# Kernel tuning notes

Hardware: AMD Instinct MI355X
Metric: run time of the kernel (lower is better)

## Reference

```python
import jax, jax.numpy as jnp
import numpy as np

N_QUBITS = 12
DIM = 2 ** N_QUBITS
N_RES_LAYERS = 3
N_HEADS = 2
N_ATTN_LAYERS = 2
SEQ_LEN = 64
HORIZON = 4
BATCH = 8
N_PARAMS = N_QUBITS * 2 * N_ATTN_LAYERS  # 48
FEAT = N_QUBITS * N_HEADS  # 24

# ---- static (numpy) precomputed gate structures (little-endian, qiskit convention) ----
_idx = np.arange(DIM)

def _cx_perm(c, t):
    # CNOT: flip target bit where control bit is 1 -> index permutation
    return np.where(((_idx >> c) & 1) == 1, _idx ^ (1 << t), _idx)

def _cz_phase(a, b):
    return (1.0 - 2.0 * (((_idx >> a) & 1) * ((_idx >> b) & 1))).astype(np.float32)

CX_LADDER = [jnp.asarray(_cx_perm(i, i + 1)) for i in range(N_QUBITS - 1)]
CX_RING = jnp.asarray(_cx_perm(N_QUBITS - 1, 0))
CX_LONG = jnp.asarray(_cx_perm(0, N_QUBITS - 1))
_CZ = []
for _layer in range(N_RES_LAYERS):
    _ph = np.ones(DIM, np.float32)
    for _i in range(_layer % 2, N_QUBITS - 1, 2):
        _ph *= _cz_phase(_i, _i + 1)
    _CZ.append(jnp.asarray(_ph))
# Qiskit Pauli label 'I'*i + 'Z' + 'I'*(n-i-1) acts on qubit n-1-i (big-endian labels)
Z_SIGNS = jnp.asarray(np.stack([
    (1.0 - 2.0 * ((_idx >> (N_QUBITS - 1 - i)) & 1)).astype(np.float32)
    for i in range(N_QUBITS)]))  # (n, DIM)


def _apply_1q(state, gate, q):
    # state: (..., DIM); gate: (2,2) or (...,2,2) broadcastable against leading dims
    hi = DIM >> (q + 1)
    lo = 1 << q
    s = state.reshape(state.shape[:-1] + (hi, 2, lo))
    out = jnp.einsum('...ij,...hjl->...hil', gate, s)
    return out.reshape(state.shape)


def _ry(theta):
    c = jnp.cos(theta / 2)
    s = jnp.sin(theta / 2)
    g = jnp.stack([jnp.stack([c, -s], -1), jnp.stack([s, c], -1)], -2)
    return g.astype(jnp.complex64)


def _rz(phi):
    em = jnp.exp(-0.5j * phi)
    ep = jnp.exp(0.5j * phi)
    z = jnp.zeros_like(em)
    return jnp.stack([jnp.stack([em, z], -1), jnp.stack([z, ep], -1)], -2)


def _u3(t, p, l):
    ct = jnp.cos(t / 2).astype(jnp.complex64)
    st = jnp.sin(t / 2).astype(jnp.complex64)
    return jnp.stack([jnp.stack([ct, -jnp.exp(1j * l) * st]),
                      jnp.stack([jnp.exp(1j * p) * st, jnp.exp(1j * (p + l)) * ct])])


def _encode_reservoir(x, res_params):
    # x: (B,T) normalized scalars -> batched statevectors (B,T,DIM)
    B, T = x.shape
    # H^{\otimes n} |0...0> = uniform superposition
    state = jnp.full((B, T, DIM), 1.0 / np.sqrt(DIM), jnp.complex64)
    for i in range(N_QUBITS):
        state = _apply_1q(state, _ry(x * np.pi * (i + 1) / N_QUBITS), i)
        state = _apply_1q(state, _rz(x * np.pi / (i + 1)), i)
    for p in CX_LADDER:
        state = state[..., p]
    state = state[..., CX_RING]
    # fixed random reservoir
    for layer in range(N_RES_LAYERS):
        for i in range(N_QUBITS):
            g = _u3(res_params[layer, i, 0], res_params[layer, i, 1], res_params[layer, i, 2])
            state = _apply_1q(state, g, i)
        state = state * _CZ[layer]
        state = state[..., CX_LONG]  # n > 2
    return state


def _project(state, params):
    # projection circuit: per layer RY/RZ on each qubit then CNOT ladder; then <Z_i>
    for layer in range(N_ATTN_LAYERS):
        for i in range(N_QUBITS):
            k = (layer * N_QUBITS + i) * 2
            state = _apply_1q(state, _ry(params[k]), i)
            state = _apply_1q(state, _rz(params[k + 1]), i)
        for p in CX_LADDER:
            state = state[..., p]
    probs = state.real ** 2 + state.imag ** 2  # (B,T,DIM)
    return jnp.einsum('btd,qd->btq', probs, Z_SIGNS)  # (B,T,n)


def setup_inputs() -> dict:
    key = jax.random.key(0)
    ks = jax.random.split(key, 6)
    sequence = jax.random.uniform(ks[0], (BATCH, SEQ_LEN), jnp.float32)
    res_params = jax.random.uniform(ks[1], (N_RES_LAYERS, N_QUBITS, 3), jnp.float32,
                                    minval=0.0, maxval=2.0 * np.pi)
    head_params = jax.random.uniform(ks[2], (N_HEADS, 3, N_PARAMS), jnp.float32,
                                     minval=0.0, maxval=2.0 * np.pi)
    W1 = jax.random.normal(ks[3], (FEAT, 2 * FEAT), jnp.float32) / np.sqrt(FEAT)
    b1 = jnp.zeros((2 * FEAT,), jnp.float32)
    W2 = jax.random.normal(ks[4], (2 * FEAT, HORIZON), jnp.float32) / np.sqrt(2 * FEAT)
    b2 = jnp.zeros((HORIZON,), jnp.float32)
    return {'sequence': sequence, 'res_params': res_params, 'head_params': head_params,
            'W1': W1, 'b1': b1, 'W2': W2, 'b2': b2}


def reference(sequence, res_params, head_params, W1, b1, W2, b2):
    states = _encode_reservoir(sequence, res_params)  # (B,T,DIM)
    T = sequence.shape[1]
    mask = jnp.triu(jnp.full((T, T), -1e9, jnp.float32), k=1)
    outs = []
    for h in range(N_HEADS):
        Q = _project(states, head_params[h, 0])
        K = _project(states, head_params[h, 1])
        V = _project(states, head_params[h, 2])
        scores = jnp.einsum('btd,bsd->bts', Q, K) / np.sqrt(N_QUBITS) + mask
        attn = jax.nn.softmax(scores, axis=-1)
        outs.append(jnp.einsum('bts,bsd->btd', attn, V))
    feats = jnp.concatenate(outs, -1)  # (B,T,FEAT)
    last = feats[:, -1, :]
    hdn = jax.nn.gelu(last @ W1 + b1, approximate=False)  # torch GELU default = exact erf
    pred = hdn @ W2 + b2  # (B, HORIZON)
    return pred
```

## Files before the change

### kernel.cpp

```cpp
#include <hip/hip_runtime.h>
#include <hip/hip_bf16.h>


#define PADDED 4224
#define HPAD   2112

#define LDSFENCE asm volatile("s_waitcnt lgkmcnt(0)" ::: "memory")

__device__ __forceinline__ int PD(int j) { return j + (j >> 5); }
__device__ __forceinline__ int PH(int i) { return i + (i >> 5); }

__device__ __forceinline__ int mapIdx(int j, int mode) {
  if (mode == 1) { int k = j ^ ((j >> 11) & 1); return k ^ ((k & 0x7FF) << 1); }
  if (mode == 2) { return j ^ ((j & 1) << 11); }
  if (mode == 3) { return j ^ ((j & 0x7FF) << 1); }
  return j;
}

template <int L>
__device__ __forceinline__ int layoutIdx(int tid, int r) {
  if constexpr (L == 0) return (tid << 4) | r;
  else if constexpr (L == 1) return ((tid & 0xF0) << 4) | (r << 4) | (tid & 15);
  else if constexpr (L == 2) return (r << 8) | tid;
  else return ((tid & 15) << 8) | (tid & 0xF0) | r;
}

template <int B>
__device__ __forceinline__ int dropbit(int j) {
  constexpr int lo = (1 << B) - 1;
  return (j & lo) | ((j >> 1) & ~lo);
}

template <int L>
__device__ __forceinline__ void ldsRead16(const float* sR, const float* sI, int tid, int mode,
                                          float ar[16], float ai[16]) {
#pragma unroll
  for (int r = 0; r < 16; ++r) {
    int j = layoutIdx<L>(tid, r);
    int a = PD(mapIdx(j, mode));
    ar[r] = sR[a]; ai[r] = sI[a];
  }
}

template <int L>
__device__ __forceinline__ void ldsWrite16(float* sR, float* sI, int tid,
                                           const float ar[16], const float ai[16], int czmask) {
#pragma unroll
  for (int r = 0; r < 16; ++r) {
    int j = layoutIdx<L>(tid, r);
    float vr = ar[r], vi = ai[r];
    if (czmask) {
      float sg = (__popc((j & (j >> 1)) & czmask) & 1) ? -1.0f : 1.0f;
      vr *= sg; vi *= sg;
    }
    int a = PD(j);
    sR[a] = vr; sI[a] = vi;
  }
}

template <int L, int B>
__device__ __forceinline__ void hWrite16(float* hR, float* hI, int tid,
                                         const float ar[16], const float ai[16]) {
#pragma unroll
  for (int r = 0; r < 16; ++r) {
    int j = layoutIdx<L>(tid, r);
    int a = PH(dropbit<B>(j));
    hR[a] = ar[r]; hI[a] = ai[r];
  }
}

template <int L, int B, int MODE>
__device__ __forceinline__ void hRead16(const float* hR, const float* hI, int tid,
                                        float ar[16], float ai[16]) {
#pragma unroll
  for (int r = 0; r < 16; ++r) {
    int j = mapIdx(layoutIdx<L>(tid, r), MODE);
    int a = PH(dropbit<B>(j));
    ar[r] = hR[a]; ai[r] = hI[a];
  }
}

__device__ __forceinline__ void applyU34(float ar[16], float ai[16], const float (*ut)[8]) {
#pragma unroll
  for (int b = 0; b < 4; ++b) {
    const float* u = ut[b];
    float u00r = u[0];
    float u01r = u[2], u01i = u[3];
    float u10r = u[4], u10i = u[5], u11r = u[6], u11i = u[7];
#pragma unroll
    for (int m = 0; m < 8; ++m) {
      int p0 = ((m >> b) << (b + 1)) | (m & ((1 << b) - 1));
      int p1 = p0 | (1 << b);
      float x0r = ar[p0], x0i = ai[p0], x1r = ar[p1], x1i = ai[p1];
      ar[p0] = u00r * x0r + u01r * x1r - u01i * x1i;
      ai[p0] = u00r * x0i + u01r * x1i + u01i * x1r;
      ar[p1] = u10r * x0r - u10i * x0i + u11r * x1r - u11i * x1i;
      ai[p1] = u10r * x0i + u10i * x0r + u11r * x1i + u11i * x1r;
    }
  }
}

__device__ __forceinline__ void applyRyRz4(float ar[16], float ai[16], const float4* gt) {
#pragma unroll
  for (int b = 0; b < 4; ++b) {
    float4 g = gt[b];
    float c = g.x, s = g.y, zr = g.z, zi = g.w;
#pragma unroll
    for (int m = 0; m < 8; ++m) {
      int p0 = ((m >> b) << (b + 1)) | (m & ((1 << b) - 1));
      int p1 = p0 | (1 << b);
      float x0r = ar[p0], x0i = ai[p0], x1r = ar[p1], x1i = ai[p1];
      float n0r = c * x0r - s * x1r;
      float n0i = c * x0i - s * x1i;
      float wr  = s * x0r + c * x1r;
      float wi  = s * x0i + c * x1i;
      ar[p0] = n0r;              ai[p0] = n0i;
      ar[p1] = wr * zr - wi * zi; ai[p1] = wr * zi + wi * zr;
    }
  }
}

template <int L>
__device__ __forceinline__ void encPass(float* sR, float* sI, int tid, int mode,
                                        const float (*ut)[8], int czmask) {
  float ar[16], ai[16];
  ldsRead16<L>(sR, sI, tid, mode, ar, ai);
  if (mode != 0) __syncthreads();
  applyU34(ar, ai, ut);
  ldsWrite16<L>(sR, sI, tid, ar, ai, czmask);
  __syncthreads();
}

template <int L>
__device__ __forceinline__ void projPass(float* sR, float* sI, int tid, int mode, const float4* gt) {
  float ar[16], ai[16];
  ldsRead16<L>(sR, sI, tid, mode, ar, ai);
  if (mode != 0) __syncthreads();
  applyRyRz4(ar, ai, gt);
  ldsWrite16<L>(sR, sI, tid, ar, ai, 0);
  __syncthreads();
}

__device__ __forceinline__ void projFinal(const float* sR, const float* sI, int tid,
                                          const float4* gt, float feat[12]) {
  float ar[16], ai[16];
#pragma unroll
  for (int r = 0; r < 16; ++r) {
    int a = PD((r << 8) | tid);
    ar[r] = sR[a]; ai[r] = sI[a];
  }
  applyRyRz4(ar, ai, gt);
  float sp = 0.f, f0 = 0.f, f1 = 0.f, f2 = 0.f, f3 = 0.f;
  int pt = __popc(tid) & 1;
#pragma unroll
  for (int r = 0; r < 16; ++r) {
    float p = ar[r] * ar[r] + ai[r] * ai[r];
    sp += p;
    int tr = r ^ (r << 1); tr ^= (tr << 2);
    f0 += ((pt ^ ((tr >> 3) & 1)) ? -p : p);
    f1 += ((pt ^ ((tr >> 2) & 1)) ? -p : p);
    f2 += ((pt ^ ((tr >> 1) & 1)) ? -p : p);
    f3 += ((pt ^ (tr & 1)) ? -p : p);
  }
  feat[0] = f0; feat[1] = f1; feat[2] = f2; feat[3] = f3;
  int tt = tid ^ (tid << 1); tt ^= (tt << 2); tt ^= (tt << 4);
#pragma unroll
  for (int q = 4; q < 12; ++q)
    feat[q] = ((tt >> (11 - q)) & 1) ? -sp : sp;
}

__device__ __forceinline__ float waveReduce(float v) {
#pragma unroll
  for (int off = 32; off; off >>= 1) v += __shfl_xor(v, off, 64);
  return v;
}


__device__ __forceinline__ void buildQtab(float4* qtab, int tid, float x) {
  const float PI = 3.14159265358979323846f;
  const float RS2 = 0.70710678118654752440f;
  if (tid < 12) {
    int i = tid;
    float th = x * PI * (float)(i + 1) / 12.0f;
    float ph = x * PI / (float)(i + 1);
    float s, c;  sincosf(0.5f * th, &s, &c);
    float zi, zr; sincosf(0.5f * ph, &zi, &zr);
    float k0 = (c - s) * RS2, k1 = (c + s) * RS2;
    qtab[i] = make_float4(k0 * zr, -k0 * zi, k1 * zr, k1 * zi);
  }
}

__device__ __forceinline__ void buildUtab(float (*utab)[8], int tid, const float* resp) {
  if (tid >= 64 && tid < 100) {
    int i = tid - 64;
    const float* rp = resp + i * 3;
    float st, ct;  sincosf(0.5f * rp[0], &st, &ct);
    float sp2, cp; sincosf(rp[1], &sp2, &cp);
    float sl, cl;  sincosf(rp[2], &sl, &cl);
    float spl, cpl; sincosf(rp[1] + rp[2], &spl, &cpl);
    float* u = utab[i];
    u[0] = ct;       u[1] = 0.0f;
    u[2] = -cl * st; u[3] = -sl * st;
    u[4] = cp * st;  u[5] = sp2 * st;
    u[6] = cpl * ct; u[7] = spl * ct;
  }
}

__device__ __forceinline__ void initProduct(float* sRe, float* sIm, int tid, const float4* qtab) {
  float pr, pi;
  {
    float4 g = qtab[4];
    int sb = tid & 1;
    pr = sb ? g.z : g.x; pi = sb ? g.w : g.y;
  }
#pragma unroll
  for (int q = 5; q < 12; ++q) {
    float4 g = qtab[q];
    int sb = (tid >> (q - 4)) & 1;
    float fr = sb ? g.z : g.x, fi = sb ? g.w : g.y;
    float nr = pr * fr - pi * fi;
    pi = pr * fi + pi * fr; pr = nr;
  }
  float4 g0 = qtab[0], g1 = qtab[1], g2 = qtab[2], g3 = qtab[3];
  float c01r[4], c01i[4], c23r[4], c23i[4];
#pragma unroll
  for (int i2 = 0; i2 < 4; ++i2) {
    float f0r = (i2 & 1) ? g0.z : g0.x, f0i = (i2 & 1) ? g0.w : g0.y;
    float f1r = (i2 & 2) ? g1.z : g1.x, f1i = (i2 & 2) ? g1.w : g1.y;
    c01r[i2] = f0r * f1r - f0i * f1i; c01i[i2] = f0r * f1i + f0i * f1r;
    float f2r = (i2 & 1) ? g2.z : g2.x, f2i = (i2 & 1) ? g2.w : g2.y;
    float f3r = (i2 & 2) ? g3.z : g3.x, f3i = (i2 & 2) ? g3.w : g3.y;
    c23r[i2] = f2r * f3r - f2i * f3i; c23i[i2] = f2r * f3i + f2i * f3r;
  }
#pragma unroll
  for (int r = 0; r < 16; ++r) {
    float lr = c01r[r & 3] * c23r[r >> 2] - c01i[r & 3] * c23i[r >> 2];
    float li = c01r[r & 3] * c23i[r >> 2] + c01i[r & 3] * c23r[r >> 2];
    int a = PD((tid << 4) | r);
    sRe[a] = pr * lr - pi * li;
    sIm[a] = pr * li + pi * lr;
  }
}

__device__ __forceinline__ void buildPtab(float4* ptab, int tid, const float* hp) {
  if (tid < 24) {
    int k = tid * 2;
    float s, c;  sincosf(0.5f * hp[k], &s, &c);
    float zi, zr; sincosf(hp[k + 1], &zi, &zr);
    ptab[tid] = make_float4(c, s, zr, zi);
  }
}


__global__ __launch_bounds__(256, 2) void enc_kernel(
    const float* __restrict__ seq, const float* __restrict__ resp,
    float* __restrict__ wsStates) {
  __shared__ float sRe[PADDED], sIm[PADDED];
  __shared__ float4 qtab[12];
  __shared__ float utab[36][8];

  const int tid = threadIdx.x;
  const int blk = blockIdx.x;
  const float x = seq[blk];

  buildQtab(qtab, tid, x);
  buildUtab(utab, tid, resp);
  __syncthreads();

  initProduct(sRe, sIm, tid, qtab);
  __syncthreads();

  encPass<0>(sRe, sIm, tid, 1, &utab[0], 0);
  encPass<1>(sRe, sIm, tid, 0, &utab[4], 0);
  encPass<2>(sRe, sIm, tid, 0, &utab[8], 0x555);
  encPass<0>(sRe, sIm, tid, 2, &utab[12], 0);
  encPass<1>(sRe, sIm, tid, 0, &utab[16], 0);
  encPass<2>(sRe, sIm, tid, 0, &utab[20], 0x2AA);
  encPass<0>(sRe, sIm, tid, 2, &utab[24], 0);
  encPass<1>(sRe, sIm, tid, 0, &utab[28], 0);

  {
    float ar[16], ai[16];
    ldsRead16<2>(sRe, sIm, tid, 0, ar, ai);
    applyU34(ar, ai, &utab[32]);
    float* gR = wsStates + (size_t)blk * 8192;
    float* gI = gR + 4096;
#pragma unroll
    for (int r = 0; r < 16; ++r) {
      int j = (r << 8) | tid;
      float sg = (__popc((j & (j >> 1)) & 0x555) & 1) ? -1.0f : 1.0f;
      int g = j ^ ((j & 1) << 11);
      gR[g] = sg * ar[r];
      gI[g] = sg * ai[r];
    }
  }
}

__global__ __launch_bounds__(256, 5) void proj_split(
    const float* __restrict__ wsStates, const float* __restrict__ hparams,
    float* __restrict__ featBase) {
  __shared__ float hRe[HPAD], hIm[HPAD];
  __shared__ float4 ptab[24];
  __shared__ float red[4][12];

  const int tid = threadIdx.x;
  const int bid = blockIdx.x;
  int h, which, s;
  if (bid < 2048) { s = bid >> 2; int pp = bid & 3; h = pp >> 1; which = 1 + (pp & 1); }
  else            { int i = bid - 2048; h = i & 1; s = (((i >> 1) << 6) | 63); which = 0; }
  const int b = s >> 6, t = s & 63;

  buildPtab(ptab, tid, hparams + (h * 3 + which) * 48);

  float ar[16], ai[16];
  const float4* pR = (const float4*)(wsStates + (size_t)s * 8192 + (tid << 4));
  const float4* pI = (const float4*)(wsStates + (size_t)s * 8192 + 4096 + (tid << 4));
#pragma unroll
  for (int k = 0; k < 4; ++k) {
    float4 vr = pR[k], vi = pI[k];
    ar[4 * k] = vr.x; ar[4 * k + 1] = vr.y; ar[4 * k + 2] = vr.z; ar[4 * k + 3] = vr.w;
    ai[4 * k] = vi.x; ai[4 * k + 1] = vi.y; ai[4 * k + 2] = vi.z; ai[4 * k + 3] = vi.w;
  }
  __syncthreads();

  const int ph7 = (tid >> 7) & 1;
  const int ph3 = (tid >> 3) & 1;
  const int ph0 = tid & 1;

  applyRyRz4(ar, ai, &ptab[0]);

  if (ph7 == 0) { hWrite16<0, 11>(hRe, hIm, tid, ar, ai); LDSFENCE; hRead16<1, 11, 0>(hRe, hIm, tid, ar, ai); }
  __syncthreads();
  if (ph7 == 1) { hWrite16<0, 11>(hRe, hIm, tid, ar, ai); LDSFENCE; hRead16<1, 11, 0>(hRe, hIm, tid, ar, ai); }

  applyRyRz4(ar, ai, &ptab[4]);

  __syncthreads();
  if (ph3 == 0) hWrite16<1, 3>(hRe, hIm, tid, ar, ai);
  __syncthreads();
  if (ph3 == 0) hRead16<2, 3, 0>(hRe, hIm, tid, ar, ai);
  __syncthreads();
  if (ph3 == 1) hWrite16<1, 3>(hRe, hIm, tid, ar, ai);
  __syncthreads();
  if (ph3 == 1) hRead16<2, 3, 0>(hRe, hIm, tid, ar, ai);

  applyRyRz4(ar, ai, &ptab[8]);

  __syncthreads();
  if (ph0 == 0) hWrite16<2, 0>(hRe, hIm, tid, ar, ai);
  __syncthreads();
  if (ph0 == 0) hRead16<1, 0, 3>(hRe, hIm, tid, ar, ai);
  __syncthreads();
  if (ph0 == 1) hWrite16<2, 0>(hRe, hIm, tid, ar, ai);
  __syncthreads();
  if (ph0 == 1) hRead16<1, 0, 3>(hRe, hIm, tid, ar, ai);

  applyRyRz4(ar, ai, &ptab[16]);

  __syncthreads();
  if (ph3 == 0) hWrite16<1, 3>(hRe, hIm, tid, ar, ai);
  __syncthreads();
  if (ph3 == 0) hRead16<2, 3, 0>(hRe, hIm, tid, ar, ai);
  __syncthreads();
  if (ph3 == 1) hWrite16<1, 3>(hRe, hIm, tid, ar, ai);
  __syncthreads();
  if (ph3 == 1) hRead16<2, 3, 0>(hRe, hIm, tid, ar, ai);

  applyRyRz4(ar, ai, &ptab[20]);

  __syncthreads();
  if (ph7 == 0) { hWrite16<2, 7>(hRe, hIm, tid, ar, ai); LDSFENCE; hRead16<3, 7, 0>(hRe, hIm, tid, ar, ai); }
  __syncthreads();
  if (ph7 == 1) { hWrite16<2, 7>(hRe, hIm, tid, ar, ai); LDSFENCE; hRead16<3, 7, 0>(hRe, hIm, tid, ar, ai); }

  applyRyRz4(ar, ai, &ptab[12]);
  float A = 0.f, B2 = 0.f, B1 = 0.f, B0 = 0.f;
#pragma unroll
  for (int r = 0; r < 16; ++r) {
    float p = ar[r] * ar[r] + ai[r] * ai[r];
    int tr = r ^ (r << 1); tr ^= (tr << 2);
    A  += ((tr >> 3) & 1) ? -p : p;
    B2 += ((tr >> 2) & 1) ? -p : p;
    B1 += ((tr >> 1) & 1) ? -p : p;
    B0 += ((tr & 1)      ) ? -p : p;
  }
  int t03p = __popc(tid & 0x0F) & 1;
  int t47p = __popc(tid & 0xF0) & 1;
  int u4   = (tid >> 4) & 1;
  int u45  = u4 ^ ((tid >> 5) & 1);
  int u456 = u45 ^ ((tid >> 6) & 1);
  int v0   = tid & 1;
  int v01  = v0 ^ ((tid >> 1) & 1);
  int v012 = v01 ^ ((tid >> 2) & 1);
  float feat[12];
  feat[0]  = (t47p ^ t03p) ? -A : A;
  feat[1]  = (t47p ^ v012) ? -A : A;
  feat[2]  = (t47p ^ v01)  ? -A : A;
  feat[3]  = (t47p ^ v0)   ? -A : A;
  feat[4]  = t47p ? -A : A;
  feat[5]  = u456 ? -A : A;
  feat[6]  = u45  ? -A : A;
  feat[7]  = u4   ? -A : A;
  feat[8]  = A;
  feat[9]  = B2;
  feat[10] = B1;
  feat[11] = B0;

#pragma unroll
  for (int q = 0; q < 12; ++q) feat[q] = waveReduce(feat[q]);
  int wid = tid >> 6;
  if ((tid & 63) == 0) {
#pragma unroll
    for (int q = 0; q < 12; ++q) red[wid][q] = feat[q];
  }
  __syncthreads();
  if (tid < 12) {
    float v = red[0][tid] + red[1][tid] + red[2][tid] + red[3][tid];
    float* dst;
    if (which == 1)      dst = featBase + (((h << 3) + b) * 64 + t) * 12;
    else if (which == 2) dst = featBase + 12288 + (((h << 3) + b) * 64 + t) * 12;
    else                 dst = featBase + 24576 + ((h << 3) + b) * 12;
    dst[tid] = v;
  }
}


__global__ __launch_bounds__(256, 2) void qstates_mono(
    const float* __restrict__ seq, const float* __restrict__ resp,
    const float* __restrict__ hparams, float* __restrict__ featBase) {
  __shared__ float sRe[PADDED], sIm[PADDED];
  __shared__ float4 qtab[12];
  __shared__ float utab[36][8];
  __shared__ float4 ptab[24];
  __shared__ float red[4][12];

  const int tid = threadIdx.x;
  const int blk = blockIdx.x;
  const int b = blk >> 6;
  const int t = blk & 63;
  const float x = seq[blk];

  buildQtab(qtab, tid, x);
  buildUtab(utab, tid, resp);
  __syncthreads();
  initProduct(sRe, sIm, tid, qtab);
  __syncthreads();

  for (int l = 0; l < 3; ++l) {
    int czm = (l & 1) ? 0x2AA : 0x555;
    encPass<0>(sRe, sIm, tid, (l == 0) ? 1 : 2, &utab[l * 12], 0);
    encPass<1>(sRe, sIm, tid, 0, &utab[l * 12 + 4], 0);
    encPass<2>(sRe, sIm, tid, 0, &utab[l * 12 + 8], czm);
  }

  float encR[16], encI[16];
#pragma unroll
  for (int r = 0; r < 16; ++r) {
    int j = (tid << 4) | r;
    int a = PD(j ^ ((j & 1) << 11));
    encR[r] = sRe[a]; encI[r] = sIm[a];
  }

  const int nproj = (t == 63) ? 6 : 4;
  for (int pj = 0; pj < nproj; ++pj) {
    int h, which;
    if (pj < 4) { h = pj >> 1; which = (pj & 1) ? 2 : 1; }
    else        { h = pj - 4;  which = 0; }
    buildPtab(ptab, tid, hparams + (h * 3 + which) * 48);
    __syncthreads();

    float ar[16], ai[16];
#pragma unroll
    for (int r = 0; r < 16; ++r) { ar[r] = encR[r]; ai[r] = encI[r]; }
    applyRyRz4(ar, ai, &ptab[0]);
    ldsWrite16<0>(sRe, sIm, tid, ar, ai, 0);
    __syncthreads();
    projPass<1>(sRe, sIm, tid, 0, &ptab[4]);
    projPass<2>(sRe, sIm, tid, 0, &ptab[8]);
    projPass<0>(sRe, sIm, tid, 3, &ptab[12]);
    projPass<1>(sRe, sIm, tid, 0, &ptab[16]);

    float feat[12];
    projFinal(sRe, sIm, tid, &ptab[20], feat);
#pragma unroll
    for (int q = 0; q < 12; ++q) feat[q] = waveReduce(feat[q]);
    int wid = tid >> 6;
    if ((tid & 63) == 0) {
#pragma unroll
      for (int q = 0; q < 12; ++q) red[wid][q] = feat[q];
    }
    __syncthreads();
    if (tid < 12) {
      float v = red[0][tid] + red[1][tid] + red[2][tid] + red[3][tid];
      float* dst;
      if (which == 1)      dst = featBase + (((h << 3) + b) * 64 + t) * 12;
      else if (which == 2) dst = featBase + 12288 + (((h << 3) + b) * 64 + t) * 12;
      else                 dst = featBase + 24576 + ((h << 3) + b) * 12;
      dst[tid] = v;
    }
    __syncthreads();
  }
}


__global__ __launch_bounds__(64) void qhead_kernel(
    const float* __restrict__ featBase,
    const float* __restrict__ W1, const float* __restrict__ b1,
    const float* __restrict__ W2, const float* __restrict__ b2,
    float* __restrict__ out) {
  __shared__ float feats[24];
  __shared__ float hdn[48];
  const int b = blockIdx.x;
  const int lane = threadIdx.x;
  const float* Kf = featBase;
  const float* Vf = featBase + 12288;
  const float* Qf = featBase + 24576;
  for (int h = 0; h < 2; ++h) {
    const float* q  = Qf + ((h << 3) + b) * 12;
    const float* kr = Kf + ((((h << 3) + b) << 6) + lane) * 12;
    float dot = 0.f;
#pragma unroll
    for (int d = 0; d < 12; ++d) dot += q[d] * kr[d];
    dot *= 0.288675134594812882f;
    float mx = dot;
#pragma unroll
    for (int off = 32; off; off >>= 1) mx = fmaxf(mx, __shfl_xor(mx, off, 64));
    float e = expf(dot - mx);
    float se = e;
#pragma unroll
    for (int off = 32; off; off >>= 1) se += __shfl_xor(se, off, 64);
    float a = e / se;
    const float* vr = Vf + ((((h << 3) + b) << 6) + lane) * 12;
#pragma unroll
    for (int d = 0; d < 12; ++d) {
      float v = a * vr[d];
#pragma unroll
      for (int off = 32; off; off >>= 1) v += __shfl_xor(v, off, 64);
      if (lane == 0) feats[h * 12 + d] = v;
    }
  }
  __syncthreads();
  if (lane < 48) {
    float acc = b1[lane];
#pragma unroll
    for (int f = 0; f < 24; ++f) acc += feats[f] * W1[f * 48 + lane];
    hdn[lane] = 0.5f * acc * (1.0f + erff(acc * 0.70710678118654752440f));
  }
  __syncthreads();
  if (lane < 4) {
    float acc = b2[lane];
#pragma unroll
    for (int k = 0; k < 48; ++k) acc += hdn[k] * W2[k * 4 + lane];
    out[(b << 2) | lane] = acc;
  }
}

extern "C" void kernel_launch(void* const* d_in, const int* in_sizes, int n_in,
                              void* d_out, int out_size, void* d_ws, size_t ws_size,
                              hipStream_t stream) {
  const float* seq     = (const float*)d_in[0];
  const float* resp    = (const float*)d_in[1];
  const float* hparams = (const float*)d_in[2];
  const float* W1      = (const float*)d_in[3];
  const float* b1      = (const float*)d_in[4];
  const float* W2      = (const float*)d_in[5];
  const float* b2      = (const float*)d_in[6];
  float* out = (float*)d_out;
  float* ws  = (float*)d_ws;

  const size_t needSplit = ((size_t)512 * 8192 + 24768) * sizeof(float);
  if (ws_size >= needSplit) {
    float* wsStates = ws;
    float* featBase = ws + (size_t)512 * 8192;
    hipLaunchKernelGGL(enc_kernel, dim3(512), dim3(256), 0, stream, seq, resp, wsStates);
    hipLaunchKernelGGL(proj_split, dim3(2064), dim3(256), 0, stream, wsStates, hparams, featBase);
    hipLaunchKernelGGL(qhead_kernel, dim3(8), dim3(64), 0, stream, featBase, W1, b1, W2, b2, out);
  } else {
    hipLaunchKernelGGL(qstates_mono, dim3(512), dim3(256), 0, stream, seq, resp, hparams, ws);
    hipLaunchKernelGGL(qhead_kernel, dim3(8), dim3(64), 0, stream, ws, W1, b1, W2, b2, out);
  }
}
```

Baseline: 165.8 us.

## Use 512 threads with 3-qubit passes in reservoir encoding kernel

```diff
diff --git a/kernel.cpp b/kernel.cpp
--- a/kernel.cpp
+++ b/kernel.cpp
@@ -25,6 +25,14 @@
   else return ((tid & 15) << 8) | (tid & 0xF0) | r;
 }
 
+template <int K>
+__device__ __forceinline__ int layoutIdx3(int tid, int r) {
+  constexpr int S = 3 * K;
+  int lo = tid & ((1 << S) - 1);
+  int hi = tid >> S;
+  return (hi << (S + 3)) | (r << S) | lo;
+}
+
 template <int B>
 __device__ __forceinline__ int dropbit(int j) {
   constexpr int lo = (1 << B) - 1;
@@ -89,6 +97,26 @@
     float u10r = u[4], u10i = u[5], u11r = u[6], u11i = u[7];
 #pragma unroll
     for (int m = 0; m < 8; ++m) {
+      int p0 = ((m >> b) << (b + 1)) | (m & ((1 << b) - 1));
+      int p1 = p0 | (1 << b);
+      float x0r = ar[p0], x0i = ai[p0], x1r = ar[p1], x1i = ai[p1];
+      ar[p0] = u00r * x0r + u01r * x1r - u01i * x1i;
+      ai[p0] = u00r * x0i + u01r * x1i + u01i * x1r;
+      ar[p1] = u10r * x0r - u10i * x0i + u11r * x1r - u11i * x1i;
+      ai[p1] = u10r * x0i + u10i * x0r + u11r * x1i + u11i * x1r;
+    }
+  }
+}
+
+__device__ __forceinline__ void applyU3_3(float ar[8], float ai[8], const float (*ut)[8]) {
+#pragma unroll
+  for (int b = 0; b < 3; ++b) {
+    const float* u = ut[b];
+    float u00r = u[0];
+    float u01r = u[2], u01i = u[3];
+    float u10r = u[4], u10i = u[5], u11r = u[6], u11i = u[7];
+#pragma unroll
+    for (int m = 0; m < 4; ++m) {
       int p0 = ((m >> b) << (b + 1)) | (m & ((1 << b) - 1));
       int p1 = p0 | (1 << b);
       float x0r = ar[p0], x0i = ai[p0], x1r = ar[p1], x1i = ai[p1];
@@ -131,13 +159,29 @@
   __syncthreads();
 }
 
-template <int L>
-__device__ __forceinline__ void projPass(float* sR, float* sI, int tid, int mode, const float4* gt) {
-  float ar[16], ai[16];
-  ldsRead16<L>(sR, sI, tid, mode, ar, ai);
+template <int K>
+__device__ __forceinline__ void encPass3(float* sR, float* sI, int tid, int mode,
+                                         const float (*ut)[8], int czmask) {
+  float ar[8], ai[8];
+#pragma unroll
+  for (int r = 0; r < 8; ++r) {
+    int j = layoutIdx3<K>(tid, r);
+    int a = PD(mapIdx(j, mode));
+    ar[r] = sR[a]; ai[r] = sI[a];
+  }
   if (mode != 0) __syncthreads();
-  applyRyRz4(ar, ai, gt);
-  ldsWrite16<L>(sR, sI, tid, ar, ai, 0);
+  applyU3_3(ar, ai, ut);
+#pragma unroll
+  for (int r = 0; r < 8; ++r) {
+    int j = layoutIdx3<K>(tid, r);
+    float vr = ar[r], vi = ai[r];
+    if (czmask) {
+      float sg = (__popc((j & (j >> 1)) & czmask) & 1) ? -1.0f : 1.0f;
+      vr *= sg; vi *= sg;
+    }
+    int a = PD(j);
+    sR[a] = vr; sI[a] = vi;
+  }
   __syncthreads();
 }
 
@@ -242,6 +286,40 @@
   }
 }
 
+__device__ __forceinline__ void initProduct3(float* sRe, float* sIm, int tid, const float4* qtab) {
+  float pr, pi;
+  {
+    float4 g = qtab[3];
+    int sb = tid & 1;
+    pr = sb ? g.z : g.x; pi = sb ? g.w : g.y;
+  }
+#pragma unroll
+  for (int q = 4; q < 12; ++q) {
+    float4 g = qtab[q];
+    int sb = (tid >> (q - 3)) & 1;
+    float fr = sb ? g.z : g.x, fi = sb ? g.w : g.y;
+    float nr = pr * fr - pi * fi;
+    pi = pr * fi + pi * fr; pr = nr;
+  }
+  float4 g0 = qtab[0], g1 = qtab[1], g2 = qtab[2];
+  float c01r[4], c01i[4];
+#pragma unroll
+  for (int i2 = 0; i2 < 4; ++i2) {
+    float f0r = (i2 & 1) ? g0.z : g0.x, f0i = (i2 & 1) ? g0.w : g0.y;
+    float f1r = (i2 & 2) ? g1.z : g1.x, f1i = (i2 & 2) ? g1.w : g1.y;
+    c01r[i2] = f0r * f1r - f0i * f1i; c01i[i2] = f0r * f1i + f0i * f1r;
+  }
+#pragma unroll
+  for (int r = 0; r < 8; ++r) {
+    float f2r = (r & 4) ? g2.z : g2.x, f2i = (r & 4) ? g2.w : g2.y;
+    float lr = c01r[r & 3] * f2r - c01i[r & 3] * f2i;
+    float li = c01r[r & 3] * f2i + c01i[r & 3] * f2r;
+    int a = PD((tid << 3) | r);
+    sRe[a] = pr * lr - pi * li;
+    sIm[a] = pr * li + pi * lr;
+  }
+}
+
 __device__ __forceinline__ void buildPtab(float4* ptab, int tid, const float* hp) {
   if (tid < 24) {
     int k = tid * 2;
@@ -252,7 +330,7 @@
 }
 
 
-__global__ __launch_bounds__(256, 2) void enc_kernel(
+__global__ __launch_bounds__(512, 4) void enc_kernel(
     const float* __restrict__ seq, const float* __restrict__ resp,
     float* __restrict__ wsStates) {
   __shared__ float sRe[PADDED], sIm[PADDED];
@@ -267,27 +345,34 @@
   buildUtab(utab, tid, resp);
   __syncthreads();
 
-  initProduct(sRe, sIm, tid, qtab);
-  __syncthreads();
-
-  encPass<0>(sRe, sIm, tid, 1, &utab[0], 0);
-  encPass<1>(sRe, sIm, tid, 0, &utab[4], 0);
-  encPass<2>(sRe, sIm, tid, 0, &utab[8], 0x555);
-  encPass<0>(sRe, sIm, tid, 2, &utab[12], 0);
-  encPass<1>(sRe, sIm, tid, 0, &utab[16], 0);
-  encPass<2>(sRe, sIm, tid, 0, &utab[20], 0x2AA);
-  encPass<0>(sRe, sIm, tid, 2, &utab[24], 0);
-  encPass<1>(sRe, sIm, tid, 0, &utab[28], 0);
+  initProduct3(sRe, sIm, tid, qtab);
+  __syncthreads();
+
+  encPass3<0>(sRe, sIm, tid, 1, &utab[0], 0);
+  encPass3<1>(sRe, sIm, tid, 0, &utab[3], 0);
+  encPass3<2>(sRe, sIm, tid, 0, &utab[6], 0);
+  encPass3<3>(sRe, sIm, tid, 0, &utab[9], 0x555);
+  encPass3<0>(sRe, sIm, tid, 2, &utab[12], 0);
+  encPass3<1>(sRe, sIm, tid, 0, &utab[15], 0);
+  encPass3<2>(sRe, sIm, tid, 0, &utab[18], 0);
+  encPass3<3>(sRe, sIm, tid, 0, &utab[21], 0x2AA);
+  encPass3<0>(sRe, sIm, tid, 2, &utab[24], 0);
+  encPass3<1>(sRe, sIm, tid, 0, &utab[27], 0);
+  encPass3<2>(sRe, sIm, tid, 0, &utab[30], 0);
 
   {
-    float ar[16], ai[16];
-    ldsRead16<2>(sRe, sIm, tid, 0, ar, ai);
-    applyU34(ar, ai, &utab[32]);
+    float ar[8], ai[8];
+#pragma unroll
+    for (int r = 0; r < 8; ++r) {
+      int a = PD((r << 9) | tid);
+      ar[r] = sRe[a]; ai[r] = sIm[a];
+    }
+    applyU3_3(ar, ai, &utab[33]);
     float* gR = wsStates + (size_t)blk * 8192;
     float* gI = gR + 4096;
 #pragma unroll
-    for (int r = 0; r < 16; ++r) {
-      int j = (r << 8) | tid;
+    for (int r = 0; r < 8; ++r) {
+      int j = (r << 9) | tid;
       float sg = (__popc((j & (j >> 1)) & 0x555) & 1) ? -1.0f : 1.0f;
       int g = j ^ ((j & 1) << 11);
       gR[g] = sg * ar[r];
@@ -475,10 +560,26 @@
     applyRyRz4(ar, ai, &ptab[0]);
     ldsWrite16<0>(sRe, sIm, tid, ar, ai, 0);
     __syncthreads();
-    projPass<1>(sRe, sIm, tid, 0, &ptab[4]);
-    projPass<2>(sRe, sIm, tid, 0, &ptab[8]);
-    projPass<0>(sRe, sIm, tid, 3, &ptab[12]);
-    projPass<1>(sRe, sIm, tid, 0, &ptab[16]);
+    {
+      float br[16], bi[16];
+      ldsRead16<1>(sRe, sIm, tid, 0, br, bi);
+      applyRyRz4(br, bi, &ptab[4]);
+      ldsWrite16<1>(sRe, sIm, tid, br, bi, 0);
+      __syncthreads();
+      ldsRead16<2>(sRe, sIm, tid, 0, br, bi);
+      applyRyRz4(br, bi, &ptab[8]);
+      ldsWrite16<2>(sRe, sIm, tid, br, bi, 0);
+      __syncthreads();
+      ldsRead16<0>(sRe, sIm, tid, 3, br, bi);
+      __syncthreads();
+      applyRyRz4(br, bi, &ptab[12]);
+      ldsWrite16<0>(sRe, sIm, tid, br, bi, 0);
+      __syncthreads();
+      ldsRead16<1>(sRe, sIm, tid, 0, br, bi);
+      applyRyRz4(br, bi, &ptab[16]);
+      ldsWrite16<1>(sRe, sIm, tid, br, bi, 0);
+      __syncthreads();
+    }
 
     float feat[12];
     projFinal(sRe, sIm, tid, &ptab[20], feat);
@@ -572,7 +673,7 @@
   if (ws_size >= needSplit) {
     float* wsStates = ws;
     float* featBase = ws + (size_t)512 * 8192;
-    hipLaunchKernelGGL(enc_kernel, dim3(512), dim3(256), 0, stream, seq, resp, wsStates);
+    hipLaunchKernelGGL(enc_kernel, dim3(512), dim3(512), 0, stream, seq, resp, wsStates);
     hipLaunchKernelGGL(proj_split, dim3(2064), dim3(256), 0, stream, wsStates, hparams, featBase);
     hipLaunchKernelGGL(qhead_kernel, dim3(8), dim3(64), 0, stream, featBase, W1, b1, W2, b2, out);
   } else {
```

Result: no change. 165.1 us (-0.4%).
